# Optimization experiments

Measured on AMD Instinct MI355X. Metric: run time of the kernel, lower is better.

## Reference

```python
import jax, jax.numpy as jnp
import numpy as np

B, L, A, D = 4, 512, 8, 256
H = 256  # hidden_dim
O = 256  # output_dim


def setup_inputs() -> dict:
    key = jax.random.key(0)
    ks = jax.random.split(key, 12)
    s = 0.05
    return {
        "x": jax.random.normal(ks[0], (B, L, A, D), dtype=jnp.float32),
        "conv_w": jax.random.normal(ks[1], (H, D), dtype=jnp.float32) * s,
        "conv_b": jax.random.normal(ks[2], (H,), dtype=jnp.float32) * s,
        "theta_w": jax.random.normal(ks[3], (H, H), dtype=jnp.float32) * s,
        "theta_b": jax.random.normal(ks[4], (H,), dtype=jnp.float32) * s,
        "phi_w": jax.random.normal(ks[5], (H, H), dtype=jnp.float32) * s,
        "phi_b": jax.random.normal(ks[6], (H,), dtype=jnp.float32) * s,
        "g_w": jax.random.normal(ks[7], (H, H), dtype=jnp.float32) * s,
        "g_b": jax.random.normal(ks[8], (H,), dtype=jnp.float32) * s,
        "f_w": jax.random.normal(ks[9], (O, H), dtype=jnp.float32) * s,
        "f_b": jax.random.normal(ks[10], (O,), dtype=jnp.float32) * s,
    }


def reference(x, conv_w, conv_b, theta_w, theta_b, phi_w, phi_b, g_w, g_b, f_w, f_b):
    batch, length, n_agents, _ = x.shape
    # residual: identity (input_dim == output_dim, stride 1)
    res = x
    # conv with kernel (1,1): pointwise projection over channel dim
    h = jnp.einsum('blad,hd->blah', x, conv_w) + conv_b  # [B,L,A,H]
    N = length * n_agents
    h = h.reshape(batch, N, H)
    theta = jnp.einsum('bnh,kh->bnk', h, theta_w) + theta_b  # [B,N,H]
    phi = jnp.einsum('bnh,kh->bnk', h, phi_w) + phi_b        # [B,N,H]
    g = jnp.einsum('bnh,kh->bnk', h, g_w) + g_b              # [B,N,H]
    scores = jnp.einsum('bnk,bmk->bnm', theta, phi) / jnp.sqrt(jnp.asarray(H, theta.dtype))
    y = jax.nn.softmax(scores, axis=2)                       # [B,N,N]
    z = jnp.einsum('bnm,bmk->bnk', y, g) / jnp.sqrt(jnp.asarray(N, y.dtype))
    out = jnp.einsum('bnk,ok->bno', z, f_w) + f_b            # [B,N,O]
    out = out.reshape(batch, length, n_agents, O)
    return out + res
```

## Files before the change

kernel.cpp:

```cpp
#include <hip/hip_runtime.h>

typedef unsigned short u16;
typedef __bf16 bf16x8 __attribute__((ext_vector_type(8)));
typedef float f32x4 __attribute__((ext_vector_type(4)));
typedef float f32x16 __attribute__((ext_vector_type(16)));
typedef float float4v __attribute__((ext_vector_type(4)));
typedef unsigned short u16x8 __attribute__((ext_vector_type(8)));
typedef unsigned short u16x4 __attribute__((ext_vector_type(4)));

#define MFMA16(a, b, c) __builtin_amdgcn_mfma_f32_16x16x32_bf16(a, b, c, 0, 0, 0)
#define MFMA32(a, b, c) __builtin_amdgcn_mfma_f32_32x32x16_bf16(a, b, c, 0, 0, 0)

__device__ __forceinline__ u16 f2bf(float f) {
  union { float f; unsigned u; } v; v.f = f;
  unsigned r = v.u + 0x7fffu + ((v.u >> 16) & 1u);
  return (u16)(r >> 16);
}
__device__ __forceinline__ float bf2f(u16 b) {
  union { unsigned u; float f; } v; v.u = ((unsigned)b) << 16;
  return v.f;
}

__device__ __forceinline__ void gload16(const void* g, void* l) {
  __builtin_amdgcn_global_load_lds(
      (__attribute__((address_space(1))) void*)g,
      (__attribute__((address_space(3))) void*)l, 16, 0, 0);
}

__device__ __forceinline__ unsigned cvtpk(float lo, float hi) {
  unsigned r;
  asm("v_cvt_pk_bf16_f32 %0, %1, %2" : "=v"(r) : "v"(lo), "v"(hi));
  return r;
}
__device__ __forceinline__ void plswap(unsigned& a, unsigned& b) {
  asm volatile("v_permlane32_swap_b32 %0, %1" : "+v"(a), "+v"(b));
}

__global__ __launch_bounds__(256) void prep_k(
    const float* __restrict__ cw, const float* __restrict__ tw,
    const float* __restrict__ pw, const float* __restrict__ gw,
    const float* __restrict__ cb, const float* __restrict__ tb,
    const float* __restrict__ pb, const float* __restrict__ gb,
    const float* __restrict__ fw,
    u16* __restrict__ Wf, float* __restrict__ biasp, u16* __restrict__ fwb) {
  const int t = threadIdx.x;
  const int bid = blockIdx.x;
  if (bid >= 768) {
    const int idx = (bid - 768) * 256 + t;
    float4v v = *(const float4v*)(fw + (size_t)idx * 4);
    u16x4 o;
#pragma unroll
    for (int i = 0; i < 4; ++i) o[i] = f2bf(v[i]);
    *(u16x4*)(fwb + (size_t)idx * 4) = o;
    return;
  }
  const int n3 = bid;
  const float* w3 = n3 < 256 ? tw + (size_t)n3 * 256
                  : n3 < 512 ? pw + (size_t)(n3 - 256) * 256
                             : gw + (size_t)(n3 - 512) * 256;
  const float b3 = n3 < 256 ? tb[n3] : n3 < 512 ? pb[n3 - 256] : gb[n3 - 512];
  __shared__ float w3s[256];
  w3s[t] = w3[t];
  __syncthreads();
  float acc = 0.0f;
#pragma unroll 8
  for (int h = 0; h < 256; ++h) acc = fmaf(w3s[h], cw[(size_t)h * 256 + t], acc);
  Wf[(size_t)n3 * 256 + t] = f2bf(acc);
  float pv = w3s[t] * cb[t];
#pragma unroll
  for (int m = 1; m < 64; m <<= 1) pv += __shfl_xor(pv, m, 64);
  __shared__ float red[4];
  if ((t & 63) == 0) red[t >> 6] = pv;
  __syncthreads();
  if (t == 0) biasp[n3] = red[0] + red[1] + red[2] + red[3] + b3;
}

__global__ __launch_bounds__(256) void gemm_tpg(
    const float* __restrict__ X, const u16* __restrict__ W,
    const float* __restrict__ bias, u16* __restrict__ Cout) {
  __shared__ u16 As[8192];
  __shared__ u16 Bs[8192];
  const int t = threadIdx.x;
  const int lane = t & 63, w = t >> 6;
  const int brow = blockIdx.x * 128, bcol = blockIdx.y * 128;
  const int wr = (w >> 1) * 64, wc = (w & 1) * 64;
  f32x4 acc[4][4];
#pragma unroll
  for (int i = 0; i < 4; ++i)
#pragma unroll
    for (int j = 0; j < 4; ++j)
#pragma unroll
      for (int r = 0; r < 4; ++r) acc[i][j][r] = 0.0f;

  const int sr = t >> 3, sc8 = (t & 7) * 8;
  const u16* gW = W + (size_t)(bcol + sr) * 256 + sc8;
  const int ar = t & 127, ach = t >> 7;
  const float* gX = X + (size_t)(brow + ar) * 256 + ach * 32;

  for (int kt = 0; kt < 256; kt += 64) {
#pragma unroll
    for (int c = 0; c < 4; ++c)
      gload16(gW + (size_t)c * 32 * 256 + kt, &Bs[c * 2048 + t * 8]);
    u16x8 pk[4];
#pragma unroll
    for (int j = 0; j < 4; ++j) {
      float4v v0 = *(const float4v*)(gX + kt + j * 8);
      float4v v1 = *(const float4v*)(gX + kt + j * 8 + 4);
#pragma unroll
      for (int e = 0; e < 4; ++e) { pk[j][e] = f2bf(v0[e]); pk[j][4 + e] = f2bf(v1[e]); }
    }
#pragma unroll
    for (int j = 0; j < 4; ++j) {
      int unit = (ach * 4 + j) ^ (ar & 7);
      *(u16x8*)(&As[ar * 64 + unit * 8]) = pk[j];
    }
    __syncthreads();
#pragma unroll
    for (int kk = 0; kk < 2; ++kk) {
      const int ko = kk * 32 + (lane >> 4) * 8;
      bf16x8 af[4], bfr[4];
#pragma unroll
      for (int i = 0; i < 4; ++i) {
        int R = wr + i * 16 + (lane & 15);
        int unit = (kk * 4 + (lane >> 4)) ^ (R & 7);
        af[i] = *(const bf16x8*)(&As[R * 64 + unit * 8]);
      }
#pragma unroll
      for (int j = 0; j < 4; ++j)
        bfr[j] = *(const bf16x8*)(&Bs[(wc + j * 16 + (lane & 15)) * 64 + ko]);
#pragma unroll
      for (int i = 0; i < 4; ++i)
#pragma unroll
        for (int j = 0; j < 4; ++j)
          acc[i][j] = MFMA16(af[i], bfr[j], acc[i][j]);
    }
    __syncthreads();
  }

  const int r0 = (lane >> 4) * 4, c0 = lane & 15;
#pragma unroll
  for (int i = 0; i < 4; ++i)
#pragma unroll
    for (int j = 0; j < 4; ++j) {
      const int col = bcol + wc + j * 16 + c0;
      const float bv = bias[col];
#pragma unroll
      for (int r = 0; r < 4; ++r) {
        const size_t o = (size_t)(brow + wr + i * 16 + r0 + r) * 768 + col;
        Cout[o] = f2bf(acc[i][j][r] + bv);
      }
    }
}

__global__ __launch_bounds__(256) void transpose_g_k(
    const u16* __restrict__ tpg, u16* __restrict__ gT) {
  __shared__ u16 T[64][65];
  const int t = threadIdx.x;
  const int bm = (blockIdx.x & 63) * 64;
  const int bk = ((blockIdx.x >> 6) & 3) * 64;
  const int b = blockIdx.x >> 8;
  const int r = t >> 3, c8 = (t & 7) * 8;
#pragma unroll
  for (int ch = 0; ch < 2; ++ch) {
    u16x8 v = *(const u16x8*)(tpg + (size_t)(b * 4096 + bm + r + ch * 32) * 768 + 512 + bk + c8);
#pragma unroll
    for (int j = 0; j < 8; ++j) T[r + ch * 32][c8 + j] = v[j];
  }
  __syncthreads();
#pragma unroll
  for (int ch = 0; ch < 2; ++ch) {
    u16x8 o;
#pragma unroll
    for (int j = 0; j < 8; ++j) o[j] = T[c8 + j][r + ch * 32];
    *(u16x8*)(gT + (size_t)(b * 256 + bk + r + ch * 32) * 4096 + bm + c8) = o;
  }
}

__global__ __launch_bounds__(256, 2) void flash2(
    const u16* __restrict__ tpg, const u16* __restrict__ gT,
    u16* __restrict__ Zp, u16* __restrict__ Lpb) {
  __shared__ u16 Kl[2][32 * 256];
  __shared__ u16 Vl[2][256 * 32];

  const int t = threadIdx.x;
  const int lane = t & 63, w = t >> 6;
  const int l31 = lane & 31, hi = lane >> 5;
  const int bid = blockIdx.x;
  const int b = bid >> 7;
  const int quarter = (bid >> 5) & 3;
  const int qt = bid & 31;
  const int q0 = qt * 128 + w * 32;
  const int kv0 = quarter * 1024;

  bf16x8 q[16];
  {
    const u16* qp = tpg + (size_t)(b * 4096 + q0 + l31) * 768 + hi * 8;
#pragma unroll
    for (int ks = 0; ks < 16; ++ks) q[ks] = *(const bf16x8*)(qp + ks * 16);
  }

  f32x16 zacc[8];
#pragma unroll
  for (int i = 0; i < 8; ++i)
#pragma unroll
    for (int j = 0; j < 16; ++j) zacc[i][j] = 0.0f;
  float ell = 0.0f;

  const int ksr = t >> 5, ksc = t & 31;

  auto stage = [&](int tile, int bi) {
    const size_t krow0 = (size_t)(b * 4096 + kv0 + tile * 32);
#pragma unroll
    for (int ch = 0; ch < 4; ++ch) {
      int r = ch * 8 + ksr;
      gload16(tpg + (krow0 + r) * 768 + 256 + ((ksc ^ r) * 8), &Kl[bi][ch * 2048 + t * 8]);
    }
#pragma unroll
    for (int ch = 0; ch < 4; ++ch) {
      int u = ch * 256 + t;
      int r = u >> 2, c16 = u & 3;
      gload16(gT + (size_t)(b * 256 + r) * 4096 + kv0 + tile * 32 + ((c16 ^ ((r >> 1) & 3)) * 8),
              &Vl[bi][u * 8]);
    }
  };

  stage(0, 0);
  __syncthreads();

  for (int tile = 0; tile < 32; ++tile) {
    const int cur = tile & 1;
    if (tile + 1 < 32) stage(tile + 1, cur ^ 1);

    f32x16 s0, s1;
#pragma unroll
    for (int j = 0; j < 16; ++j) { s0[j] = 0.0f; s1[j] = 0.0f; }
    const u16* kb = &Kl[cur][0];
    __builtin_amdgcn_s_setprio(1);
#pragma unroll
    for (int ks = 0; ks < 8; ++ks) {
      bf16x8 kfa = *(const bf16x8*)(kb + l31 * 256 + (((2 * ks + hi) ^ l31) * 8));
      bf16x8 kfb = *(const bf16x8*)(kb + l31 * 256 + (((2 * (ks + 8) + hi) ^ l31) * 8));
      s0 = MFMA32(kfa, q[ks], s0);
      s1 = MFMA32(kfb, q[ks + 8], s1);
    }
    __builtin_amdgcn_s_setprio(0);
#pragma unroll
    for (int j = 0; j < 16; ++j) s0[j] += s1[j];

    bf16x8 pa[2];
#pragma unroll
    for (int half = 0; half < 2; ++half) {
      float p[8];
#pragma unroll
      for (int g = 0; g < 8; ++g) {
        p[g] = __builtin_amdgcn_exp2f(s0[half * 8 + g] * 0.09016844f);
        ell += p[g];
      }
      unsigned x0 = cvtpk(p[0], p[1]), y0 = cvtpk(p[4], p[5]);
      unsigned x1 = cvtpk(p[2], p[3]), y1 = cvtpk(p[6], p[7]);
      plswap(x0, y0);
      plswap(x1, y1);
      union { unsigned u[4]; bf16x8 v; } cc;
      cc.u[0] = x0; cc.u[1] = x1; cc.u[2] = y0; cc.u[3] = y1;
      pa[half] = cc.v;
    }

    const u16* vb = &Vl[cur][0];
    __builtin_amdgcn_s_setprio(1);
#pragma unroll
    for (int ks2 = 0; ks2 < 2; ++ks2) {
#pragma unroll
      for (int nt = 0; nt < 8; ++nt) {
        int row = nt * 32 + l31;
        bf16x8 vv = *(const bf16x8*)(vb + row * 32 + (((2 * ks2 + hi) ^ ((row >> 1) & 3)) * 8));
        zacc[nt] = MFMA32(pa[ks2], vv, zacc[nt]);
      }
    }
    __builtin_amdgcn_s_setprio(0);
    __syncthreads();
  }

  ell += __shfl_xor(ell, 32, 64);

#pragma unroll
  for (int g = 0; g < 16; ++g) {
    int r = (g & 3) + 8 * (g >> 2) + 4 * hi;
    size_t rowoff = ((size_t)(quarter * 16384 + b * 4096 + q0 + r)) * 256 + l31;
#pragma unroll
    for (int nt = 0; nt < 8; ++nt) Zp[rowoff + nt * 32] = f2bf(zacc[nt][g]);
  }
  if (lane < 32) Lpb[quarter * 16384 + b * 4096 + q0 + l31] = f2bf(ell);
}

__global__ __launch_bounds__(256) void gemm_out(
    const u16* __restrict__ Zp, const u16* __restrict__ Lpb,
    const u16* __restrict__ W, const float* __restrict__ bias,
    float* __restrict__ Cout, const float* __restrict__ res) {
  __shared__ u16 As[8192];
  __shared__ u16 Bs[8192];
  const int t = threadIdx.x;
  const int lane = t & 63, w = t >> 6;
  const int brow = blockIdx.x * 128, bcol = blockIdx.y * 128;
  const int wr = (w >> 1) * 64, wc = (w & 1) * 64;
  f32x4 acc[4][4];
#pragma unroll
  for (int i = 0; i < 4; ++i)
#pragma unroll
    for (int j = 0; j < 4; ++j)
#pragma unroll
      for (int r = 0; r < 4; ++r) acc[i][j][r] = 0.0f;

  const int sr = t >> 3, sc8 = (t & 7) * 8;
  const u16* gW = W + (size_t)(bcol + sr) * 256 + sc8;
  const int ar = t >> 1, ach = t & 1;
  const int am = brow + ar;
  const float linv = 1.0f /
      ((bf2f(Lpb[am]) + bf2f(Lpb[16384 + am]) + bf2f(Lpb[32768 + am]) + bf2f(Lpb[49152 + am])) *
       64.0f);

  for (int kt = 0; kt < 256; kt += 64) {
#pragma unroll
    for (int c = 0; c < 4; ++c)
      gload16(gW + (size_t)c * 32 * 256 + kt, &Bs[c * 2048 + t * 8]);
    const int col0 = kt + ach * 32;
    float sacc[32];
#pragma unroll
    for (int e = 0; e < 32; ++e) sacc[e] = 0.0f;
#pragma unroll
    for (int qd = 0; qd < 4; ++qd) {
      const u16* zp = Zp + ((size_t)(qd * 16384) + am) * 256 + col0;
#pragma unroll
      for (int j = 0; j < 4; ++j) {
        u16x8 v = *(const u16x8*)(zp + j * 8);
#pragma unroll
        for (int e = 0; e < 8; ++e) sacc[j * 8 + e] += bf2f(v[e]);
      }
    }
#pragma unroll
    for (int j = 0; j < 4; ++j) {
      u16x8 pk;
#pragma unroll
      for (int e = 0; e < 8; ++e) pk[e] = f2bf(sacc[j * 8 + e] * linv);
      int unit = (ach * 4 + j) ^ (ar & 7);
      *(u16x8*)(&As[ar * 64 + unit * 8]) = pk;
    }
    __syncthreads();
#pragma unroll
    for (int kk = 0; kk < 2; ++kk) {
      const int ko = kk * 32 + (lane >> 4) * 8;
      bf16x8 af[4], bfr[4];
#pragma unroll
      for (int i = 0; i < 4; ++i) {
        int R = wr + i * 16 + (lane & 15);
        int unit = (kk * 4 + (lane >> 4)) ^ (R & 7);
        af[i] = *(const bf16x8*)(&As[R * 64 + unit * 8]);
      }
#pragma unroll
      for (int j = 0; j < 4; ++j)
        bfr[j] = *(const bf16x8*)(&Bs[(wc + j * 16 + (lane & 15)) * 64 + ko]);
#pragma unroll
      for (int i = 0; i < 4; ++i)
#pragma unroll
        for (int j = 0; j < 4; ++j)
          acc[i][j] = MFMA16(af[i], bfr[j], acc[i][j]);
    }
    __syncthreads();
  }

  const int r0 = (lane >> 4) * 4, c0 = lane & 15;
#pragma unroll
  for (int i = 0; i < 4; ++i)
#pragma unroll
    for (int j = 0; j < 4; ++j) {
      const int col = bcol + wc + j * 16 + c0;
      const float bv = bias[col];
#pragma unroll
      for (int r = 0; r < 4; ++r) {
        const size_t o = (size_t)(brow + wr + i * 16 + r0 + r) * 256 + col;
        Cout[o] = acc[i][j][r] + bv + res[o];
      }
    }
}

extern "C" void kernel_launch(void* const* d_in, const int* in_sizes, int n_in,
                              void* d_out, int out_size, void* d_ws, size_t ws_size,
                              hipStream_t stream) {
  const float* x  = (const float*)d_in[0];
  const float* cw = (const float*)d_in[1];
  const float* cb = (const float*)d_in[2];
  const float* tw = (const float*)d_in[3];
  const float* tb = (const float*)d_in[4];
  const float* pw = (const float*)d_in[5];
  const float* pb = (const float*)d_in[6];
  const float* gw = (const float*)d_in[7];
  const float* gb = (const float*)d_in[8];
  const float* fw = (const float*)d_in[9];
  const float* fb = (const float*)d_in[10];

  char* ws = (char*)d_ws;
  u16*   tpg   = (u16*)(ws);
  u16*   gT    = (u16*)(ws + 25165824);
  u16*   Zp    = (u16*)(ws + 33554432);
  u16*   Lpb   = (u16*)(ws + 67108864);
  u16*   Wf    = (u16*)(ws + 67239936);
  u16*   fwb   = (u16*)(ws + 67633152);
  float* biasp = (float*)(ws + 67764224);

  prep_k<<<832, 256, 0, stream>>>(cw, tw, pw, gw, cb, tb, pb, gb, fw, Wf, biasp, fwb);
  gemm_tpg<<<dim3(128, 6), 256, 0, stream>>>(x, Wf, biasp, tpg);
  transpose_g_k<<<1024, 256, 0, stream>>>(tpg, gT);
  flash2<<<512, 256, 0, stream>>>(tpg, gT, Zp, Lpb);
  gemm_out<<<dim3(128, 2), 256, 0, stream>>>(Zp, Lpb, fwb, fb, (float*)d_out, x);
}
```

Measured before the change: 244.1 us.

## Fold output projection into g weights and write transposed g from projection GEMM

Uses associativity to fold the output projection f_w into the g projection weights, W_g' = f_w·g_w·conv_w. Attention then produces output-space values directly, and the final GEMM becomes an elementwise merge that adds bias and residual. The projection GEMM now writes the g part straight into its transposed layout, which removes the separate transpose kernel and shrinks the tpg buffer. It also merges the two split QK accumulators into one MFMA chain. This trades a small extra weight-prep kernel and a longer dependent MFMA chain for removing one GEMM launch and one transpose pass. Strided u16x4 stores into gT may be less coalesced.

Result: faster. 218.7 us (-10.4%).

```diff
diff --git a/kernel.cpp b/kernel.cpp
--- a/kernel.cpp
+++ b/kernel.cpp
@@ -36,48 +36,65 @@
   asm volatile("v_permlane32_swap_b32 %0, %1" : "+v"(a), "+v"(b));
 }
 
-__global__ __launch_bounds__(256) void prep_k(
+__global__ __launch_bounds__(256) void prep1(
     const float* __restrict__ cw, const float* __restrict__ tw,
     const float* __restrict__ pw, const float* __restrict__ gw,
     const float* __restrict__ cb, const float* __restrict__ tb,
     const float* __restrict__ pb, const float* __restrict__ gb,
-    const float* __restrict__ fw,
-    u16* __restrict__ Wf, float* __restrict__ biasp, u16* __restrict__ fwb) {
+    u16* __restrict__ Wbig, float* __restrict__ biasp,
+    float* __restrict__ Gtmp, float* __restrict__ gvec) {
   const int t = threadIdx.x;
   const int bid = blockIdx.x;
-  if (bid >= 768) {
-    const int idx = (bid - 768) * 256 + t;
-    float4v v = *(const float4v*)(fw + (size_t)idx * 4);
-    u16x4 o;
-#pragma unroll
-    for (int i = 0; i < 4; ++i) o[i] = f2bf(v[i]);
-    *(u16x4*)(fwb + (size_t)idx * 4) = o;
-    return;
-  }
-  const int n3 = bid;
-  const float* w3 = n3 < 256 ? tw + (size_t)n3 * 256
-                  : n3 < 512 ? pw + (size_t)(n3 - 256) * 256
-                             : gw + (size_t)(n3 - 512) * 256;
-  const float b3 = n3 < 256 ? tb[n3] : n3 < 512 ? pb[n3 - 256] : gb[n3 - 512];
+  const int n3 = bid & 255;
+  const float* wsrc = bid < 256 ? tw : bid < 512 ? pw : gw;
   __shared__ float w3s[256];
-  w3s[t] = w3[t];
+  w3s[t] = wsrc[(size_t)n3 * 256 + t];
   __syncthreads();
   float acc = 0.0f;
 #pragma unroll 8
   for (int h = 0; h < 256; ++h) acc = fmaf(w3s[h], cw[(size_t)h * 256 + t], acc);
-  Wf[(size_t)n3 * 256 + t] = f2bf(acc);
   float pv = w3s[t] * cb[t];
 #pragma unroll
   for (int m = 1; m < 64; m <<= 1) pv += __shfl_xor(pv, m, 64);
   __shared__ float red[4];
   if ((t & 63) == 0) red[t >> 6] = pv;
   __syncthreads();
-  if (t == 0) biasp[n3] = red[0] + red[1] + red[2] + red[3] + b3;
+  const float dotcb = red[0] + red[1] + red[2] + red[3];
+  if (bid < 512) {
+    Wbig[(size_t)bid * 256 + t] = f2bf(acc);
+    if (t == 0) biasp[bid] = dotcb + (bid < 256 ? tb[n3] : pb[n3]);
+  } else {
+    Gtmp[(size_t)n3 * 256 + t] = acc;
+    if (t == 0) gvec[n3] = dotcb + gb[n3];
+  }
+}
+
+__global__ __launch_bounds__(256) void prep2(
+    const float* __restrict__ fw, const float* __restrict__ Gtmp,
+    const float* __restrict__ gvec, u16* __restrict__ Wbig,
+    float* __restrict__ biasp) {
+  const int t = threadIdx.x;
+  const int o = blockIdx.x;
+  __shared__ float fs[256];
+  fs[t] = fw[(size_t)o * 256 + t];
+  __syncthreads();
+  float acc = 0.0f;
+#pragma unroll 8
+  for (int h = 0; h < 256; ++h) acc = fmaf(fs[h], Gtmp[(size_t)h * 256 + t], acc);
+  Wbig[(size_t)(512 + o) * 256 + t] = f2bf(acc);
+  float pv = fs[t] * gvec[t];
+#pragma unroll
+  for (int m = 1; m < 64; m <<= 1) pv += __shfl_xor(pv, m, 64);
+  __shared__ float red[4];
+  if ((t & 63) == 0) red[t >> 6] = pv;
+  __syncthreads();
+  if (t == 0) biasp[512 + o] = red[0] + red[1] + red[2] + red[3];
 }
 
 __global__ __launch_bounds__(256) void gemm_tpg(
     const float* __restrict__ X, const u16* __restrict__ W,
-    const float* __restrict__ bias, u16* __restrict__ Cout) {
+    const float* __restrict__ bias, u16* __restrict__ tpg,
+    u16* __restrict__ gT) {
   __shared__ u16 As[8192];
   __shared__ u16 Bs[8192];
   const int t = threadIdx.x;
@@ -138,41 +155,34 @@
   }
 
   const int r0 = (lane >> 4) * 4, c0 = lane & 15;
-#pragma unroll
-  for (int i = 0; i < 4; ++i)
-#pragma unroll
-    for (int j = 0; j < 4; ++j) {
-      const int col = bcol + wc + j * 16 + c0;
-      const float bv = bias[col];
-#pragma unroll
-      for (int r = 0; r < 4; ++r) {
-        const size_t o = (size_t)(brow + wr + i * 16 + r0 + r) * 768 + col;
-        Cout[o] = f2bf(acc[i][j][r] + bv);
-      }
-    }
-}
-
-__global__ __launch_bounds__(256) void transpose_g_k(
-    const u16* __restrict__ tpg, u16* __restrict__ gT) {
-  __shared__ u16 T[64][65];
-  const int t = threadIdx.x;
-  const int bm = (blockIdx.x & 63) * 64;
-  const int bk = ((blockIdx.x >> 6) & 3) * 64;
-  const int b = blockIdx.x >> 8;
-  const int r = t >> 3, c8 = (t & 7) * 8;
-#pragma unroll
-  for (int ch = 0; ch < 2; ++ch) {
-    u16x8 v = *(const u16x8*)(tpg + (size_t)(b * 4096 + bm + r + ch * 32) * 768 + 512 + bk + c8);
-#pragma unroll
-    for (int j = 0; j < 8; ++j) T[r + ch * 32][c8 + j] = v[j];
-  }
-  __syncthreads();
-#pragma unroll
-  for (int ch = 0; ch < 2; ++ch) {
-    u16x8 o;
-#pragma unroll
-    for (int j = 0; j < 8; ++j) o[j] = T[c8 + j][r + ch * 32];
-    *(u16x8*)(gT + (size_t)(b * 256 + bk + r + ch * 32) * 4096 + bm + c8) = o;
+  if (blockIdx.y < 4) {
+#pragma unroll
+    for (int i = 0; i < 4; ++i)
+#pragma unroll
+      for (int j = 0; j < 4; ++j) {
+        const int col = bcol + wc + j * 16 + c0;
+        const float bv = bias[col];
+#pragma unroll
+        for (int r = 0; r < 4; ++r) {
+          const size_t o = (size_t)(brow + wr + i * 16 + r0 + r) * 512 + col;
+          tpg[o] = f2bf(acc[i][j][r] + bv);
+        }
+      }
+  } else {
+#pragma unroll
+    for (int i = 0; i < 4; ++i) {
+      const int m0 = brow + wr + i * 16 + r0;
+      const int b = m0 >> 12, n0 = m0 & 4095;
+#pragma unroll
+      for (int j = 0; j < 4; ++j) {
+        const int col = bcol + wc + j * 16 + c0;
+        const float bv = bias[col];
+        u16x4 ov;
+#pragma unroll
+        for (int r = 0; r < 4; ++r) ov[r] = f2bf(acc[i][j][r] + bv);
+        *(u16x4*)(gT + ((size_t)((b << 8) + (col - 512))) * 4096 + n0) = ov;
+      }
+    }
   }
 }
 
@@ -194,7 +204,7 @@
 
   bf16x8 q[16];
   {
-    const u16* qp = tpg + (size_t)(b * 4096 + q0 + l31) * 768 + hi * 8;
+    const u16* qp = tpg + (size_t)(b * 4096 + q0 + l31) * 512 + hi * 8;
 #pragma unroll
     for (int ks = 0; ks < 16; ++ks) q[ks] = *(const bf16x8*)(qp + ks * 16);
   }
@@ -213,7 +223,7 @@
 #pragma unroll
     for (int ch = 0; ch < 4; ++ch) {
       int r = ch * 8 + ksr;
-      gload16(tpg + (krow0 + r) * 768 + 256 + ((ksc ^ r) * 8), &Kl[bi][ch * 2048 + t * 8]);
+      gload16(tpg + (krow0 + r) * 512 + 256 + ((ksc ^ r) * 8), &Kl[bi][ch * 2048 + t * 8]);
     }
 #pragma unroll
     for (int ch = 0; ch < 4; ++ch) {
@@ -231,21 +241,17 @@
     const int cur = tile & 1;
     if (tile + 1 < 32) stage(tile + 1, cur ^ 1);
 
-    f32x16 s0, s1;
-#pragma unroll
-    for (int j = 0; j < 16; ++j) { s0[j] = 0.0f; s1[j] = 0.0f; }
+    f32x16 s;
+#pragma unroll
+    for (int j = 0; j < 16; ++j) s[j] = 0.0f;
     const u16* kb = &Kl[cur][0];
     __builtin_amdgcn_s_setprio(1);
 #pragma unroll
-    for (int ks = 0; ks < 8; ++ks) {
-      bf16x8 kfa = *(const bf16x8*)(kb + l31 * 256 + (((2 * ks + hi) ^ l31) * 8));
-      bf16x8 kfb = *(const bf16x8*)(kb + l31 * 256 + (((2 * (ks + 8) + hi) ^ l31) * 8));
-      s0 = MFMA32(kfa, q[ks], s0);
-      s1 = MFMA32(kfb, q[ks + 8], s1);
+    for (int ks = 0; ks < 16; ++ks) {
+      bf16x8 kf = *(const bf16x8*)(kb + l31 * 256 + (((2 * ks + hi) ^ l31) * 8));
+      s = MFMA32(kf, q[ks], s);
     }
     __builtin_amdgcn_s_setprio(0);
-#pragma unroll
-    for (int j = 0; j < 16; ++j) s0[j] += s1[j];
 
     bf16x8 pa[2];
 #pragma unroll
@@ -253,7 +259,7 @@
       float p[8];
 #pragma unroll
       for (int g = 0; g < 8; ++g) {
-        p[g] = __builtin_amdgcn_exp2f(s0[half * 8 + g] * 0.09016844f);
+        p[g] = __builtin_amdgcn_exp2f(s[half * 8 + g] * 0.09016844f);
         ell += p[g];
       }
       unsigned x0 = cvtpk(p[0], p[1]), y0 = cvtpk(p[4], p[5]);
@@ -292,94 +298,37 @@
   if (lane < 32) Lpb[quarter * 16384 + b * 4096 + q0 + l31] = f2bf(ell);
 }
 
-__global__ __launch_bounds__(256) void gemm_out(
+__global__ __launch_bounds__(256) void merge_out(
     const u16* __restrict__ Zp, const u16* __restrict__ Lpb,
-    const u16* __restrict__ W, const float* __restrict__ bias,
-    float* __restrict__ Cout, const float* __restrict__ res) {
-  __shared__ u16 As[8192];
-  __shared__ u16 Bs[8192];
-  const int t = threadIdx.x;
-  const int lane = t & 63, w = t >> 6;
-  const int brow = blockIdx.x * 128, bcol = blockIdx.y * 128;
-  const int wr = (w >> 1) * 64, wc = (w & 1) * 64;
-  f32x4 acc[4][4];
-#pragma unroll
-  for (int i = 0; i < 4; ++i)
-#pragma unroll
-    for (int j = 0; j < 4; ++j)
-#pragma unroll
-      for (int r = 0; r < 4; ++r) acc[i][j][r] = 0.0f;
-
-  const int sr = t >> 3, sc8 = (t & 7) * 8;
-  const u16* gW = W + (size_t)(bcol + sr) * 256 + sc8;
-  const int ar = t >> 1, ach = t & 1;
-  const int am = brow + ar;
-  const float linv = 1.0f /
-      ((bf2f(Lpb[am]) + bf2f(Lpb[16384 + am]) + bf2f(Lpb[32768 + am]) + bf2f(Lpb[49152 + am])) *
-       64.0f);
-
-  for (int kt = 0; kt < 256; kt += 64) {
-#pragma unroll
-    for (int c = 0; c < 4; ++c)
-      gload16(gW + (size_t)c * 32 * 256 + kt, &Bs[c * 2048 + t * 8]);
-    const int col0 = kt + ach * 32;
-    float sacc[32];
-#pragma unroll
-    for (int e = 0; e < 32; ++e) sacc[e] = 0.0f;
-#pragma unroll
-    for (int qd = 0; qd < 4; ++qd) {
-      const u16* zp = Zp + ((size_t)(qd * 16384) + am) * 256 + col0;
-#pragma unroll
-      for (int j = 0; j < 4; ++j) {
-        u16x8 v = *(const u16x8*)(zp + j * 8);
-#pragma unroll
-        for (int e = 0; e < 8; ++e) sacc[j * 8 + e] += bf2f(v[e]);
-      }
-    }
-#pragma unroll
-    for (int j = 0; j < 4; ++j) {
-      u16x8 pk;
-#pragma unroll
-      for (int e = 0; e < 8; ++e) pk[e] = f2bf(sacc[j * 8 + e] * linv);
-      int unit = (ach * 4 + j) ^ (ar & 7);
-      *(u16x8*)(&As[ar * 64 + unit * 8]) = pk;
-    }
-    __syncthreads();
-#pragma unroll
-    for (int kk = 0; kk < 2; ++kk) {
-      const int ko = kk * 32 + (lane >> 4) * 8;
-      bf16x8 af[4], bfr[4];
-#pragma unroll
-      for (int i = 0; i < 4; ++i) {
-        int R = wr + i * 16 + (lane & 15);
-        int unit = (kk * 4 + (lane >> 4)) ^ (R & 7);
-        af[i] = *(const bf16x8*)(&As[R * 64 + unit * 8]);
-      }
-#pragma unroll
-      for (int j = 0; j < 4; ++j)
-        bfr[j] = *(const bf16x8*)(&Bs[(wc + j * 16 + (lane & 15)) * 64 + ko]);
-#pragma unroll
-      for (int i = 0; i < 4; ++i)
-#pragma unroll
-        for (int j = 0; j < 4; ++j)
-          acc[i][j] = MFMA16(af[i], bfr[j], acc[i][j]);
-    }
-    __syncthreads();
-  }
-
-  const int r0 = (lane >> 4) * 4, c0 = lane & 15;
-#pragma unroll
-  for (int i = 0; i < 4; ++i)
-#pragma unroll
-    for (int j = 0; j < 4; ++j) {
-      const int col = bcol + wc + j * 16 + c0;
-      const float bv = bias[col];
-#pragma unroll
-      for (int r = 0; r < 4; ++r) {
-        const size_t o = (size_t)(brow + wr + i * 16 + r0 + r) * 256 + col;
-        Cout[o] = acc[i][j][r] + bv + res[o];
-      }
-    }
+    const float* __restrict__ fb, const float* __restrict__ x,
+    float* __restrict__ out) {
+  const int idx = blockIdx.x * 256 + threadIdx.x;
+  const int m = idx >> 5;
+  const int c = (idx & 31) * 8;
+  const float l = bf2f(Lpb[m]) + bf2f(Lpb[16384 + m]) + bf2f(Lpb[32768 + m]) +
+                  bf2f(Lpb[49152 + m]);
+  const float inv = 1.0f / (l * 64.0f);
+  float acc[8];
+#pragma unroll
+  for (int j = 0; j < 8; ++j) acc[j] = 0.0f;
+#pragma unroll
+  for (int qd = 0; qd < 4; ++qd) {
+    u16x8 v = *(const u16x8*)(Zp + ((size_t)(qd * 16384) + m) * 256 + c);
+#pragma unroll
+    for (int j = 0; j < 8; ++j) acc[j] += bf2f(v[j]);
+  }
+  const float4v fb0 = *(const float4v*)(fb + c);
+  const float4v fb1 = *(const float4v*)(fb + c + 4);
+  const float4v x0 = *(const float4v*)(x + (size_t)m * 256 + c);
+  const float4v x1 = *(const float4v*)(x + (size_t)m * 256 + c + 4);
+  float4v o0, o1;
+#pragma unroll
+  for (int j = 0; j < 4; ++j) {
+    o0[j] = acc[j] * inv + fb0[j] + x0[j];
+    o1[j] = acc[4 + j] * inv + fb1[j] + x1[j];
+  }
+  *(float4v*)(out + (size_t)m * 256 + c) = o0;
+  *(float4v*)(out + (size_t)m * 256 + c + 4) = o1;
 }
 
 extern "C" void kernel_launch(void* const* d_in, const int* in_sizes, int n_in,
@@ -399,16 +348,18 @@
 
   char* ws = (char*)d_ws;
   u16*   tpg   = (u16*)(ws);
-  u16*   gT    = (u16*)(ws + 25165824);
-  u16*   Zp    = (u16*)(ws + 33554432);
-  u16*   Lpb   = (u16*)(ws + 67108864);
-  u16*   Wf    = (u16*)(ws + 67239936);
-  u16*   fwb   = (u16*)(ws + 67633152);
-  float* biasp = (float*)(ws + 67764224);
-
-  prep_k<<<832, 256, 0, stream>>>(cw, tw, pw, gw, cb, tb, pb, gb, fw, Wf, biasp, fwb);
-  gemm_tpg<<<dim3(128, 6), 256, 0, stream>>>(x, Wf, biasp, tpg);
-  transpose_g_k<<<1024, 256, 0, stream>>>(tpg, gT);
+  u16*   gT    = (u16*)(ws + 16777216);
+  u16*   Zp    = (u16*)(ws + 25165824);
+  u16*   Lpb   = (u16*)(ws + 58720256);
+  u16*   Wbig  = (u16*)(ws + 58851328);
+  float* biasp = (float*)(ws + 59244544);
+  float* Gtmp  = (float*)(ws + 59247616);
+  float* gvec  = (float*)(ws + 59509760);
+
+  prep1<<<768, 256, 0, stream>>>(cw, tw, pw, gw, cb, tb, pb, gb,
+                                 Wbig, biasp, Gtmp, gvec);
+  prep2<<<256, 256, 0, stream>>>(fw, Gtmp, gvec, Wbig, biasp);
+  gemm_tpg<<<dim3(128, 6), 256, 0, stream>>>(x, Wbig, biasp, tpg, gT);
   flash2<<<512, 256, 0, stream>>>(tpg, gT, Zp, Lpb);
-  gemm_out<<<dim3(128, 2), 256, 0, stream>>>(Zp, Lpb, fwb, fb, (float*)d_out, x);
-}
+  merge_out<<<2048, 256, 0, stream>>>(Zp, Lpb, fb, x, (float*)d_out);
+}
```
